# Optimization experiments

Hardware: AMD Instinct MI355X
Metric: run time of the kernel (lower is better)

The kernel has to match this reference:

```python
import jax, jax.numpy as jnp
import numpy as np

INPUT_DIM = 2048
N_FORMULAS = 2048
LITERALS_PER_FORMULA = 16
TOTAL_LITERALS = N_FORMULAS * LITERALS_PER_FORMULA
BINARY_THRESHOLD_EPS = 1.0
ELASTIC_NET_BETA = 0.4


def setup_inputs() -> dict:
    key = jax.random.key(0)
    k1, k2 = jax.random.split(key, 2)
    # learnable mask: original init is eps + 0.5 everywhere; use values in [0, 2]
    # so that the binary threshold at eps=1 is exercised on both sides.
    learnable_mask = jax.random.uniform(k1, (INPUT_DIM, N_FORMULAS), jnp.float32, 0.0, 2.0)
    elastic_net_alpha = jnp.zeros((1,), jnp.float32)
    # per-formula random feature keep mask (Bernoulli, keep_feature_prob ~ 0.5)
    formulas_random_mask = (jax.random.uniform(k2, (INPUT_DIM, N_FORMULAS)) < 0.5).astype(jnp.float32)
    # sparse extension matrix represented as: literal j belongs to formula j // L
    formula_id_per_literal = (jnp.arange(TOTAL_LITERALS, dtype=jnp.int32) // LITERALS_PER_FORMULA)
    return {
        "learnable_mask": learnable_mask,
        "elastic_net_alpha": elastic_net_alpha,
        "formulas_random_mask": formulas_random_mask,
        "formula_id_per_literal": formula_id_per_literal,
    }


def binary_threshold(x, eps):
    # 1.0 where |x| > eps else 0.0 (hard threshold, zero gradient)
    return jnp.where(jnp.abs(x) > eps, jnp.float32(1.0), jnp.float32(0.0))


def reference(learnable_mask, elastic_net_alpha, formulas_random_mask, formula_id_per_literal):
    eps = BINARY_THRESHOLD_EPS
    beta = ELASTIC_NET_BETA
    # number of features kept per formula: [F]
    n_effective_features = jnp.sum(formulas_random_mask, axis=0)
    # diag(matmul(A^T, B)) == einsum('if,if->f') -- same math, no O(F^2) waste
    l2_square_norm_selected = jnp.einsum("if,if->f", jnp.square(learnable_mask), formulas_random_mask)
    l1_norm_selected = jnp.einsum("if,if->f", jnp.abs(learnable_mask), formulas_random_mask)
    l2 = jnp.abs(l2_square_norm_selected / n_effective_features - beta * eps * eps)
    l1 = jnp.abs(l1_norm_selected / n_effective_features - beta * eps)
    sig = jax.nn.sigmoid(elastic_net_alpha[0])
    elastic_net_reg = jnp.mean(l2 * ((1.0 - sig) / 2.0) + l1 * sig)
    # binarize then expand formula columns to literal columns (sparse-dense matmul
    # with a {0,1} selection matrix == column gather)
    learnable_mask_01 = binary_threshold(learnable_mask, eps)
    learnable_binary_mask = jnp.take(learnable_mask_01, formula_id_per_literal, axis=1)  # [D, L_total]
    literals_random_mask = jnp.take(formulas_random_mask, formula_id_per_literal, axis=1)  # [D, L_total]
    return learnable_binary_mask, literals_random_mask, elastic_net_reg
```

## Files before the change

### kernel.cpp

```cpp
#include <hip/hip_runtime.h>
#include <math.h>

#define DIM 2048
#define NF 2048
#define LPF 16
#define LTOT (NF * LPF)
#define BETA 0.4f
#define EPS 1.0f
#define NDCH 64
#define DCH (DIM / NDCH)

typedef float f32x4 __attribute__((ext_vector_type(4)));

__global__ void reduce_prefetch(const float* __restrict__ lm,
                                const float* __restrict__ frm,
                                float* __restrict__ ws) {
    const int f = blockIdx.x * 256 + threadIdx.x;
    const int d0 = blockIdx.y * DCH;

    float sq = 0.0f, l1 = 0.0f, cnt = 0.0f;
    #pragma unroll 8
    for (int i = 0; i < DCH; ++i) {
        const size_t off = ((size_t)(d0 + i) << 11) + f;
        float x = lm[off];
        float r = frm[off];
        sq  = fmaf(x * x, r, sq);
        l1  = fmaf(fabsf(x), r, l1);
        cnt += r;
    }

    float* w = ws + (size_t)blockIdx.y * 3 * NF;
    w[0 * NF + f] = sq;
    w[1 * NF + f] = l1;
    w[2 * NF + f] = cnt;
}

__global__ void expand_stream(const float* __restrict__ lm,
                              const float* __restrict__ frm,
                              f32x4* __restrict__ out0,
                              f32x4* __restrict__ out1) {
    const int t = threadIdx.x;
    const int bx = blockIdx.x;
    const bool is1 = bx >= DIM;
    const int d = is1 ? bx - DIM : bx;
    const float* src = is1 ? frm : lm;
    f32x4* dst = (is1 ? out1 : out0) + ((size_t)d << 13);

    const float* row = src + ((size_t)d << 11) + (t >> 2);

    float vals[32];
    #pragma unroll
    for (int i = 0; i < 32; ++i)
        vals[i] = __builtin_nontemporal_load(&row[i * 64]);

    if (!is1) {
        #pragma unroll
        for (int i = 0; i < 32; ++i)
            vals[i] = (fabsf(vals[i]) > EPS) ? 1.0f : 0.0f;
    }

    #pragma unroll
    for (int i = 0; i < 32; ++i) {
        f32x4 q = { vals[i], vals[i], vals[i], vals[i] };
        dst[i * 256 + t] = q;
    }
}

__global__ void formula_term_kernel(const float* __restrict__ ws,
                                    const float* __restrict__ alpha,
                                    float* __restrict__ ws2) {
    const int f = blockIdx.x * blockDim.x + threadIdx.x;
    float sig = 1.0f / (1.0f + expf(-alpha[0]));
    float w_l2 = (1.0f - sig) * 0.5f;
    float w_l1 = sig;

    float sq = 0.0f, l1 = 0.0f, cnt = 0.0f;
    for (int c = 0; c < NDCH; ++c) {
        const float* w = ws + (size_t)c * 3 * NF;
        sq  += w[0 * NF + f];
        l1  += w[1 * NF + f];
        cnt += w[2 * NF + f];
    }
    float l2t = fabsf(sq / cnt - BETA * EPS * EPS);
    float l1t = fabsf(l1 / cnt - BETA * EPS);
    ws2[f] = l2t * w_l2 + l1t * w_l1;
}

__global__ void final_sum_kernel(const float* __restrict__ ws2,
                                 float* __restrict__ out_scalar) {
    __shared__ float red[256];
    const int t = threadIdx.x;
    float total = 0.0f;
    for (int k = 0; k < NF / 256; ++k)
        total += ws2[t + k * 256];
    red[t] = total;
    __syncthreads();
    for (int s = 128; s > 0; s >>= 1) {
        if (t < s) red[t] += red[t + s];
        __syncthreads();
    }
    if (t == 0) out_scalar[0] = red[0] / (float)NF;
}

extern "C" void kernel_launch(void* const* d_in, const int* in_sizes, int n_in,
                              void* d_out, int out_size, void* d_ws, size_t ws_size,
                              hipStream_t stream) {
    const float* lm    = (const float*)d_in[0];
    const float* alpha = (const float*)d_in[1];
    const float* frm   = (const float*)d_in[2];

    float* out = (float*)d_out;
    float* ws  = (float*)d_ws;

    const size_t big = (size_t)DIM * LTOT;
    f32x4* out0 = (f32x4*)out;
    f32x4* out1 = (f32x4*)(out + big);
    float* out_scalar = out + 2 * big;
    float* ws2 = ws + (size_t)NDCH * 3 * NF;

    dim3 gridA(NF / 256, NDCH);
    reduce_prefetch<<<gridA, 256, 0, stream>>>(lm, frm, ws);

    expand_stream<<<2 * DIM, 256, 0, stream>>>(lm, frm, out0, out1);

    formula_term_kernel<<<NF / 256, 256, 0, stream>>>(ws, alpha, ws2);
    final_sum_kernel<<<1, 256, 0, stream>>>(ws2, out_scalar);
}
```

Before: 134.9 us.

## Bit-pack thresholded masks in the reduction pass and expand from bits

The reduction kernel now builds 64-bit wave ballots of the thresholded learnable mask and of the random mask for every row. It stores these packed words in workspace. The expand kernel then reads those compact bit words instead of re-reading both full float matrices, removing roughly 32MB of redundant global reads from the write-bound expansion. In exchange the reduction pass does extra ballots and small stores. The random-mask output is reconstructed from a >0.5 test, so it assumes that mask holds only 0/1 values.

```diff
diff --git a/kernel.cpp b/kernel.cpp
--- a/kernel.cpp
+++ b/kernel.cpp
@@ -11,22 +11,36 @@
 #define DCH (DIM / NDCH)
 
 typedef float f32x4 __attribute__((ext_vector_type(4)));
+typedef unsigned long long u64;
 
-__global__ void reduce_prefetch(const float* __restrict__ lm,
-                                const float* __restrict__ frm,
-                                float* __restrict__ ws) {
-    const int f = blockIdx.x * 256 + threadIdx.x;
+__global__ void reduce_pack(const float* __restrict__ lm,
+                            const float* __restrict__ frm,
+                            float* __restrict__ ws,
+                            u64* __restrict__ pack_lm,
+                            u64* __restrict__ pack_fr) {
+    const int t = threadIdx.x;
+    const int f = blockIdx.x * 256 + t;
     const int d0 = blockIdx.y * DCH;
+    const int wv = t >> 6;
+    const int lane = t & 63;
 
     float sq = 0.0f, l1 = 0.0f, cnt = 0.0f;
-    #pragma unroll 8
+    #pragma unroll 4
     for (int i = 0; i < DCH; ++i) {
-        const size_t off = ((size_t)(d0 + i) << 11) + f;
+        const int d = d0 + i;
+        const size_t off = ((size_t)d << 11) + f;
         float x = lm[off];
         float r = frm[off];
         sq  = fmaf(x * x, r, sq);
         l1  = fmaf(fabsf(x), r, l1);
         cnt += r;
+        u64 bl = __ballot(fabsf(x) > EPS);
+        u64 br = __ballot(r > 0.5f);
+        if (lane == 0) {
+            const size_t widx = (size_t)d * 32 + blockIdx.x * 4 + wv;
+            pack_lm[widx] = bl;
+            pack_fr[widx] = br;
+        }
     }
 
     float* w = ws + (size_t)blockIdx.y * 3 * NF;
@@ -35,33 +49,27 @@
     w[2 * NF + f] = cnt;
 }
 
-__global__ void expand_stream(const float* __restrict__ lm,
-                              const float* __restrict__ frm,
-                              f32x4* __restrict__ out0,
-                              f32x4* __restrict__ out1) {
+__global__ void expand_pure(const u64* __restrict__ pack_lm,
+                            const u64* __restrict__ pack_fr,
+                            f32x4* __restrict__ out0,
+                            f32x4* __restrict__ out1) {
     const int t = threadIdx.x;
     const int bx = blockIdx.x;
     const bool is1 = bx >= DIM;
     const int d = is1 ? bx - DIM : bx;
-    const float* src = is1 ? frm : lm;
+    const u64* pack = (is1 ? pack_fr : pack_lm) + (size_t)d * 32;
     f32x4* dst = (is1 ? out1 : out0) + ((size_t)d << 13);
+    const unsigned sh = t >> 2;
 
-    const float* row = src + ((size_t)d << 11) + (t >> 2);
-
-    float vals[32];
+    u64 w[32];
     #pragma unroll
     for (int i = 0; i < 32; ++i)
-        vals[i] = __builtin_nontemporal_load(&row[i * 64]);
-
-    if (!is1) {
-        #pragma unroll
-        for (int i = 0; i < 32; ++i)
-            vals[i] = (fabsf(vals[i]) > EPS) ? 1.0f : 0.0f;
-    }
+        w[i] = pack[i];
 
     #pragma unroll
     for (int i = 0; i < 32; ++i) {
-        f32x4 q = { vals[i], vals[i], vals[i], vals[i] };
+        float v = ((w[i] >> sh) & 1ull) ? 1.0f : 0.0f;
+        f32x4 q = { v, v, v, v };
         dst[i * 256 + t] = q;
     }
 }
@@ -116,12 +124,15 @@
     f32x4* out0 = (f32x4*)out;
     f32x4* out1 = (f32x4*)(out + big);
     float* out_scalar = out + 2 * big;
+
     float* ws2 = ws + (size_t)NDCH * 3 * NF;
+    u64* pack_lm = (u64*)(ws2 + NF);
+    u64* pack_fr = pack_lm + (size_t)DIM * 32;
 
     dim3 gridA(NF / 256, NDCH);
-    reduce_prefetch<<<gridA, 256, 0, stream>>>(lm, frm, ws);
+    reduce_pack<<<gridA, 256, 0, stream>>>(lm, frm, ws, pack_lm, pack_fr);
 
-    expand_stream<<<2 * DIM, 256, 0, stream>>>(lm, frm, out0, out1);
+    expand_pure<<<2 * DIM, 256, 0, stream>>>(pack_lm, pack_fr, out0, out1);
 
     formula_term_kernel<<<NF / 256, 256, 0, stream>>>(ws, alpha, ws2);
     final_sum_kernel<<<1, 256, 0, stream>>>(ws2, out_scalar);
```

Measured after the change: 135.8 us. No clear change (+0.6%).
